# Optimization experiments

Hardware: AMD Instinct MI355X
Metric: run time of the kernel (lower is better)

Reference implementation:

```python
import jax, jax.numpy as jnp
import numpy as np

N, E, F_IN, H, L, G, C = 50000, 640000, 128, 128, 3, 256, 10
NEG_SLOPE = 0.2  # PyG GATConv default leaky_relu slope


def setup_inputs() -> dict:
    key = jax.random.key(0)
    ks = jax.random.split(key, 10)
    x = jax.random.normal(ks[0], (N, F_IN), jnp.float32)
    edge_index = jax.random.randint(ks[1], (2, E), 0, N, dtype=jnp.int32)
    # sorted graph ids covering all G graphs (global_max_pool segments)
    batch = (jnp.arange(N, dtype=jnp.int32) * G) // N
    s = 1.0 / np.sqrt(H)
    # 3 GAT layers all map 128->128 (F_IN == H), so stack their params
    Wc = jax.random.normal(ks[2], (L, F_IN, H), jnp.float32) * s
    a_src = jax.random.normal(ks[3], (L, H), jnp.float32) * s
    a_dst = jax.random.normal(ks[4], (L, H), jnp.float32) * s
    bc = jnp.zeros((L, H), jnp.float32)
    W1 = jax.random.normal(ks[5], (H, H), jnp.float32) * s
    b1 = jnp.zeros((H,), jnp.float32)
    W2 = jax.random.normal(ks[6], (H, C), jnp.float32) * s
    b2 = jnp.zeros((C,), jnp.float32)
    return dict(x=x, edge_index=edge_index, batch=batch, Wc=Wc, a_src=a_src,
                a_dst=a_dst, bc=bc, W1=W1, b1=b1, W2=W2, b2=b2)


def _gat_layer(h_in, W, a_s, a_d, b, src, dst):
    h = h_in @ W                                   # [N, H]
    e_s = (h * a_s).sum(-1)                        # [N] source term
    e_d = (h * a_d).sum(-1)                        # [N] target term
    e = jax.nn.leaky_relu(e_s[src] + e_d[dst], NEG_SLOPE)  # [E']
    # softmax over incoming edges of each target node
    m = jax.ops.segment_max(e, dst, num_segments=N)
    w = jnp.exp(e - m[dst])
    z = jax.ops.segment_sum(w, dst, num_segments=N)
    alpha = w / (z[dst] + 1e-16)
    out = jax.ops.segment_sum(alpha[:, None] * h[src], dst, num_segments=N)
    return out + b


def reference(x, edge_index, batch, Wc, a_src, a_dst, bc, W1, b1, W2, b2):
    loops = jnp.arange(N, dtype=edge_index.dtype)  # GATConv adds self-loops
    src = jnp.concatenate([edge_index[0], loops])
    dst = jnp.concatenate([edge_index[1], loops])
    h = x
    for l in range(L):
        h = jax.nn.relu(_gat_layer(h, Wc[l], a_src[l], a_dst[l], bc[l], src, dst))
    g = jax.ops.segment_max(h, batch, num_segments=G)  # global_max_pool [G, H]
    g = jax.nn.relu(g @ W1 + b1)
    logits = g @ W2 + b2
    return jax.nn.log_softmax(logits, axis=-1)
```

## Files before the change

### kernel.cpp

```cpp
#include <hip/hip_runtime.h>
#include <hip/hip_fp16.h>
#include <math.h>

#define N_ 50000
#define E_ 640000
#define H_ 128
#define L_ 3
#define G_ 256
#define C_ 10
#define NEG_SLOPE 0.2f

#define ABLK ((N_ + 3) / 4)
#define MAXDEG 64
#define GEMM_BLKS ((N_ + 63) / 64)
#define FILL_T (GEMM_BLKS * 256)

typedef _Float16 half8 __attribute__((ext_vector_type(8)));
typedef float f32x4 __attribute__((ext_vector_type(4)));

__device__ __forceinline__ float leaky(float x) { return x > 0.f ? x : NEG_SLOPE * x; }
__device__ __forceinline__ int pi_out(int p) { return ((p & 7) << 4) + (p >> 3); }

__device__ __forceinline__ void prep_layer(int l, const float* __restrict__ Wc,
                                           const float* __restrict__ a_src,
                                           const float* __restrict__ a_dst,
                                           const float* __restrict__ bc,
                                           __half* __restrict__ Wt,
                                           float* __restrict__ bcp) {
    const float* W = Wc + l * 16384;
    __half* T = Wt + (size_t)l * 144 * 128;
    int t = threadIdx.x;
    for (int e = t; e < 16384; e += 256) {
        int n = e >> 7, p = e & 127;
        int ks = (l == 0) ? p : pi_out(p);
        T[n * 128 + p] = __float2half(W[ks * 128 + n]);
    }
    if (t < 128) {
        int p = t;
        int ks = (l == 0) ? p : pi_out(p);
        const float* as = a_src + l * 128;
        const float* ad = a_dst + l * 128;
        float s = 0.f, d = 0.f;
#pragma unroll 8
        for (int n = 0; n < 128; n++) {
            float w = W[ks * 128 + n];
            s += w * as[n];
            d += w * ad[n];
        }
        T[128 * 128 + p] = __float2half(s);
        T[129 * 128 + p] = __float2half(d);
        bcp[l * 128 + p] = bc[l * 128 + pi_out(p)];
    } else {
        int kk = t - 128;
        for (int r = 130; r < 144; r++) T[r * 128 + kk] = __float2half(0.f);
    }
}

__global__ __launch_bounds__(256) void zero_prep(int* __restrict__ cur,
                                                 const float* __restrict__ Wc,
                                                 const float* __restrict__ a_src,
                                                 const float* __restrict__ a_dst,
                                                 const float* __restrict__ bc,
                                                 __half* __restrict__ Wt,
                                                 float* __restrict__ bcp) {
    if (blockIdx.x < L_) {
        prep_layer(blockIdx.x, Wc, a_src, a_dst, bc, Wt, bcp);
    } else {
        int i = (blockIdx.x - L_) * 256 + threadIdx.x;
        if (i < N_) cur[i] = 0;
    }
}

__global__ __launch_bounds__(256) void gemm0_fill(const float* __restrict__ A,
                                                  const __half* __restrict__ Wt,
                                                  __half* __restrict__ h16,
                                                  float* __restrict__ es,
                                                  float* __restrict__ ed,
                                                  const int* __restrict__ src,
                                                  const int* __restrict__ dst,
                                                  int* __restrict__ cur,
                                                  int* __restrict__ col_slots) {
    __shared__ __half Bsw[144 * 128];
    int tid = threadIdx.x;
    int brow = blockIdx.x * 64;
    int w = tid >> 6, l = tid & 63;
    int lrow = l & 15, lk = l >> 4;

    int g = blockIdx.x * 256 + tid;
    int e1 = g + FILL_T, e2 = g + 2 * FILL_T, e3 = g + 3 * FILL_T;
    bool v3 = e3 < E_;
    int d0 = dst[g], d1 = dst[e1], d2 = dst[e2];
    int s0 = src[g], s1 = src[e1], s2 = src[e2];
    int d3 = 0, s3 = 0;
    if (v3) { d3 = dst[e3]; s3 = src[e3]; }

    int p0 = atomicAdd(&cur[d0], 1);
    int p1 = atomicAdd(&cur[d1], 1);
    int p2 = atomicAdd(&cur[d2], 1);
    int p3 = MAXDEG;
    if (v3) p3 = atomicAdd(&cur[d3], 1);

    int arow = brow + w * 16 + lrow;
    float4 av[8];
    if (arow < N_) {
        const float4* rp = (const float4*)(A + (size_t)arow * 128);
#pragma unroll
        for (int kk = 0; kk < 4; kk++) {
            av[2 * kk]     = rp[kk * 8 + lk * 2];
            av[2 * kk + 1] = rp[kk * 8 + lk * 2 + 1];
        }
    } else {
        float4 zz = make_float4(0.f, 0.f, 0.f, 0.f);
#pragma unroll
        for (int s = 0; s < 8; s++) av[s] = zz;
    }

    {
        const float4* srcW = (const float4*)Wt;
#pragma unroll
        for (int i = 0; i < 9; i++) {
            int c = tid + i * 256;
            int o = c * 16;
            int n = o >> 8;
            float4 val = srcW[c];
            int addr = n * 256 + ((o & 255) ^ ((n & 7) << 4));
            *(float4*)((char*)Bsw + addr) = val;
        }
    }
    __syncthreads();

    f32x4 acc[9];
#pragma unroll
    for (int t = 0; t < 9; t++) acc[t] = (f32x4)0.f;
#pragma unroll
    for (int kk = 0; kk < 4; kk++) {
        half8 af;
        float4 a0 = av[2 * kk], a1 = av[2 * kk + 1];
        af[0] = (_Float16)a0.x; af[1] = (_Float16)a0.y; af[2] = (_Float16)a0.z; af[3] = (_Float16)a0.w;
        af[4] = (_Float16)a1.x; af[5] = (_Float16)a1.y; af[6] = (_Float16)a1.z; af[7] = (_Float16)a1.w;
        int kbyte = kk * 64 + lk * 16;
#pragma unroll
        for (int t = 0; t < 9; t++) {
            int n = t * 16 + lrow;
            half8 bf = *(const half8*)((const char*)Bsw + n * 256 + (kbyte ^ ((n & 7) << 4)));
            acc[t] = __builtin_amdgcn_mfma_f32_16x16x32_f16(af, bf, acc[t], 0, 0, 0);
        }
    }

    int row0 = brow + w * 16 + lk * 4;
#pragma unroll
    for (int rr = 0; rr < 4; rr++) {
        int gr = row0 + rr;
        if (gr < N_) {
            half8 hv;
#pragma unroll
            for (int t = 0; t < 8; t++) hv[t] = (_Float16)acc[t][rr];
            *(half8*)(h16 + (size_t)gr * 128 + lrow * 8) = hv;
            if (lrow == 0) es[gr] = acc[8][rr];
            else if (lrow == 1) ed[gr] = acc[8][rr];
        }
    }

    if (p0 < MAXDEG) col_slots[d0 * MAXDEG + p0] = s0;
    if (p1 < MAXDEG) col_slots[d1 * MAXDEG + p1] = s1;
    if (p2 < MAXDEG) col_slots[d2 * MAXDEG + p2] = s2;
    if (p3 < MAXDEG) col_slots[d3 * MAXDEG + p3] = s3;
}

__global__ __launch_bounds__(256) void gemm_mfma(const __half* __restrict__ Ah,
                                                 const __half* __restrict__ Wt,
                                                 __half* __restrict__ h16,
                                                 float* __restrict__ es,
                                                 float* __restrict__ ed) {
    __shared__ __half Bsw[144 * 128];
    int tid = threadIdx.x;
    int brow = blockIdx.x * 64;
    int w = tid >> 6, l = tid & 63;
    int lrow = l & 15, lk = l >> 4;

    int arow = brow + w * 16 + lrow;
    half8 afr[4];
    if (arow < N_) {
        const char* rb = (const char*)(Ah + (size_t)arow * 128);
#pragma unroll
        for (int kk = 0; kk < 4; kk++)
            afr[kk] = *(const half8*)(rb + kk * 64 + lk * 16);
    } else {
#pragma unroll
        for (int kk = 0; kk < 4; kk++) afr[kk] = (half8)(_Float16)0.f;
    }

    {
        const float4* srcW = (const float4*)Wt;
#pragma unroll
        for (int i = 0; i < 9; i++) {
            int c = tid + i * 256;
            int o = c * 16;
            int n = o >> 8;
            float4 val = srcW[c];
            int addr = n * 256 + ((o & 255) ^ ((n & 7) << 4));
            *(float4*)((char*)Bsw + addr) = val;
        }
    }
    __syncthreads();

    f32x4 acc[9];
#pragma unroll
    for (int t = 0; t < 9; t++) acc[t] = (f32x4)0.f;
#pragma unroll
    for (int kk = 0; kk < 4; kk++) {
        int kbyte = kk * 64 + lk * 16;
#pragma unroll
        for (int t = 0; t < 9; t++) {
            int n = t * 16 + lrow;
            half8 bf = *(const half8*)((const char*)Bsw + n * 256 + (kbyte ^ ((n & 7) << 4)));
            acc[t] = __builtin_amdgcn_mfma_f32_16x16x32_f16(afr[kk], bf, acc[t], 0, 0, 0);
        }
    }

    int row0 = brow + w * 16 + lk * 4;
#pragma unroll
    for (int rr = 0; rr < 4; rr++) {
        int gr = row0 + rr;
        if (gr < N_) {
            half8 hv;
#pragma unroll
            for (int t = 0; t < 8; t++) hv[t] = (_Float16)acc[t][rr];
            *(half8*)(h16 + (size_t)gr * 128 + lrow * 8) = hv;
            if (lrow == 0) es[gr] = acc[8][rr];
            else if (lrow == 1) ed[gr] = acc[8][rr];
        }
    }
}

__global__ __launch_bounds__(256) void gat_aggregate(const __half* __restrict__ h16,
                                                     const float* __restrict__ es,
                                                     const float* __restrict__ ed,
                                                     const int* __restrict__ cur,
                                                     const int* __restrict__ col_slots,
                                                     const float* __restrict__ biasp,
                                                     __half* __restrict__ hout) {
    __shared__ int   lds_s[4][64];
    __shared__ float lds_w[4][64];
    int wv = threadIdx.x >> 6;
    int lane = threadIdx.x & 63;
    int node = blockIdx.x * 4 + wv;
    if (node >= N_) return;

    int deg_raw = cur[node];
    int craw = col_slots[node * MAXDEG + lane];
    float edn = ed[node];
    float es_self = es[node];

    int deg = min(deg_raw, MAXDEG);
    int c0 = (lane < deg) ? min(max(craw, 0), N_ - 1) : node;
    lds_s[wv][lane] = c0;

    float w0 = 0.f;
    if (lane < deg) w0 = __expf(fminf(leaky(es[c0] + edn), 30.f));
    float zl = w0;
    lds_w[wv][lane] = w0;

    int eg = lane >> 4;
    int fl = lane & 15;

    float acc[8] = {0.f, 0.f, 0.f, 0.f, 0.f, 0.f, 0.f, 0.f};
    int K4 = (deg + 15) >> 4;
    for (int b = 0; b < K4; ++b) {
        int jb = eg + (b << 4);
        int s0 = lds_s[wv][jb];
        int s1 = lds_s[wv][jb + 4];
        int s2 = lds_s[wv][jb + 8];
        int s3 = lds_s[wv][jb + 12];
        float a0 = lds_w[wv][jb];
        float a1 = lds_w[wv][jb + 4];
        float a2 = lds_w[wv][jb + 8];
        float a3 = lds_w[wv][jb + 12];
        union { float4 f4; __half2 h2[4]; } u0, u1, u2, u3;
        u0.f4 = *(const float4*)(h16 + (size_t)s0 * 128 + fl * 8);
        u1.f4 = *(const float4*)(h16 + (size_t)s1 * 128 + fl * 8);
        u2.f4 = *(const float4*)(h16 + (size_t)s2 * 128 + fl * 8);
        u3.f4 = *(const float4*)(h16 + (size_t)s3 * 128 + fl * 8);
#pragma unroll
        for (int qq = 0; qq < 4; qq++) {
            float2 f0 = __half22float2(u0.h2[qq]);
            float2 f1 = __half22float2(u1.h2[qq]);
            float2 f2 = __half22float2(u2.h2[qq]);
            float2 f3 = __half22float2(u3.h2[qq]);
            acc[2 * qq]     += a0 * f0.x + a1 * f1.x + a2 * f2.x + a3 * f3.x;
            acc[2 * qq + 1] += a0 * f0.y + a1 * f1.y + a2 * f2.y + a3 * f3.y;
        }
    }

#pragma unroll
    for (int qq = 0; qq < 8; qq++) {
        acc[qq] += __shfl_xor(acc[qq], 16);
        acc[qq] += __shfl_xor(acc[qq], 32);
    }
#pragma unroll
    for (int o = 32; o; o >>= 1) zl += __shfl_xor(zl, o);
    float ws = __expf(fminf(leaky(es_self + edn), 30.f));
    float inv = 1.0f / (zl + ws + 1e-16f);

    if (eg == 0) {
        union { float4 f4; __half2 h2[4]; } su;
        su.f4 = *(const float4*)(h16 + (size_t)node * 128 + fl * 8);
        const float4* bp = (const float4*)(biasp + fl * 8);
        float4 b0 = bp[0], b1 = bp[1];
        float bq[8] = {b0.x, b0.y, b0.z, b0.w, b1.x, b1.y, b1.z, b1.w};
        union { float4 f4; __half2 h2[4]; } ou;
#pragma unroll
        for (int qq = 0; qq < 4; qq++) {
            float2 sv = __half22float2(su.h2[qq]);
            float v0 = fmaxf((acc[2 * qq]     + ws * sv.x) * inv + bq[2 * qq],     0.f);
            float v1 = fmaxf((acc[2 * qq + 1] + ws * sv.y) * inv + bq[2 * qq + 1], 0.f);
            ou.h2[qq] = __floats2half2_rn(v0, v1);
        }
        *(float4*)(hout + (size_t)node * 128 + fl * 8) = ou.f4;
    }
}

__device__ __forceinline__ int lower_bound_batch(const int* __restrict__ batch, int val) {
    int lo = 0, hi = N_;
    while (lo < hi) {
        int mid = (lo + hi) >> 1;
        if (batch[mid] < val) lo = mid + 1;
        else hi = mid;
    }
    return lo;
}

__global__ __launch_bounds__(512) void pool_head(const __half* __restrict__ h16,
                                                 const int* __restrict__ batch,
                                                 const float* __restrict__ W1,
                                                 const float* __restrict__ b1,
                                                 const float* __restrict__ W2,
                                                 const float* __restrict__ b2,
                                                 float* __restrict__ out) {
    int g = blockIdx.x;
    int t = threadIdx.x;
    __shared__ float red[8][128];
    __shared__ float gs[128], gp[128], lg[C_], lse;

    int s = lower_bound_batch(batch, g);
    int e = lower_bound_batch(batch, g + 1);
    int fs = t & 15;
    int rg = t >> 4;
    float m[8] = {0.f, 0.f, 0.f, 0.f, 0.f, 0.f, 0.f, 0.f};
    for (int i = s + rg; i < e; i += 32) {
        union { float4 f4; __half2 h2[4]; } u;
        u.f4 = *(const float4*)(h16 + (size_t)i * 128 + fs * 8);
#pragma unroll
        for (int qq = 0; qq < 4; qq++) {
            float2 fv = __half22float2(u.h2[qq]);
            m[2 * qq]     = fmaxf(m[2 * qq],     fv.x);
            m[2 * qq + 1] = fmaxf(m[2 * qq + 1], fv.y);
        }
    }
#pragma unroll
    for (int qq = 0; qq < 8; qq++) {
        m[qq] = fmaxf(m[qq], __shfl_xor(m[qq], 16));
        m[qq] = fmaxf(m[qq], __shfl_xor(m[qq], 32));
    }
    int wid = t >> 6;
    if ((t & 48) == 0) {
#pragma unroll
        for (int qq = 0; qq < 8; qq++) red[wid][fs * 8 + qq] = m[qq];
    }
    __syncthreads();
    if (t < 128) {
        float mm = red[0][t];
#pragma unroll
        for (int w = 1; w < 8; w++) mm = fmaxf(mm, red[w][t]);
        gs[t] = mm;
    }
    __syncthreads();

    if (t < 128) {
        float acc = b1[t];
#pragma unroll 8
        for (int k = 0; k < 128; k++) {
            int f = pi_out(k);
            acc += gs[k] * W1[f * 128 + t];
        }
        gp[t] = fmaxf(acc, 0.f);
    }
    __syncthreads();
    if (t < C_) {
        float a2 = b2[t];
#pragma unroll 8
        for (int k = 0; k < 128; k++) a2 += gp[k] * W2[k * C_ + t];
        lg[t] = a2;
    }
    __syncthreads();
    if (t == 0) {
        float mm = lg[0];
#pragma unroll
        for (int i = 1; i < C_; i++) mm = fmaxf(mm, lg[i]);
        float ss = 0.f;
#pragma unroll
        for (int i = 0; i < C_; i++) ss += expf(lg[i] - mm);
        lse = mm + logf(ss);
    }
    __syncthreads();
    if (t < C_) out[g * C_ + t] = lg[t] - lse;
}

extern "C" void kernel_launch(void* const* d_in, const int* in_sizes, int n_in,
                              void* d_out, int out_size, void* d_ws, size_t ws_size,
                              hipStream_t stream) {
    const float* x     = (const float*)d_in[0];
    const int*   eidx  = (const int*)d_in[1];
    const int*   batch = (const int*)d_in[2];
    const float* Wc    = (const float*)d_in[3];
    const float* a_src = (const float*)d_in[4];
    const float* a_dst = (const float*)d_in[5];
    const float* bc    = (const float*)d_in[6];
    const float* W1    = (const float*)d_in[7];
    const float* b1    = (const float*)d_in[8];
    const float* W2    = (const float*)d_in[9];
    const float* b2    = (const float*)d_in[10];
    float* out = (float*)d_out;

    const int* srcs = eidx;
    const int* dsts = eidx + E_;

    __half* hG16  = (__half*)d_ws;
    __half* hB16  = hG16 + (size_t)N_ * 128;
    float*  es    = (float*)(hB16 + (size_t)N_ * 128);
    float*  ed    = es + N_;
    float*  bcp   = ed + N_;
    __half* Wt    = (__half*)(bcp + 3 * 128);
    int*    cur       = (int*)(Wt + (size_t)3 * 144 * 128);
    int*    col_slots = cur + N_;

    zero_prep<<<L_ + (N_ + 255) / 256, 256, 0, stream>>>(cur, Wc, a_src, a_dst, bc, Wt, bcp);

    gemm0_fill<<<GEMM_BLKS, 256, 0, stream>>>(x, Wt, hG16, es, ed,
                                              srcs, dsts, cur, col_slots);

    gat_aggregate<<<ABLK, 256, 0, stream>>>(hG16, es, ed, cur, col_slots, bcp, hB16);
    for (int l = 1; l < L_; ++l) {
        gemm_mfma<<<GEMM_BLKS, 256, 0, stream>>>(
            hB16, Wt + (size_t)l * 144 * 128, hG16, es, ed);
        gat_aggregate<<<ABLK, 256, 0, stream>>>(hG16, es, ed, cur, col_slots,
                                                bcp + l * 128, hB16);
    }

    pool_head<<<G_, 512, 0, stream>>>(hB16, batch, W1, b1, W2, b2, out);
}
```

Baseline: 186.0 us.

## Fuse GAT aggregation with next layer's MFMA GEMM via LDS tile

Layers 0 and 1 now run their edge-softmax aggregation (plus bias and ReLU) inside the following layer's GEMM kernel. Each 64-node tile is aggregated into LDS, then multiplied by the next weight matrix with MFMA. This removes a global write and read of the intermediate fp16 activations and one kernel launch per fused pair. The es/ed buffers are double-buffered so one launch can read the old attention terms while writing the new ones. The cost is fewer, heavier blocks (64 nodes each instead of 4) and more LDS use, which may lower occupancy for the gather-heavy phase.

```diff
diff --git a/kernel.cpp b/kernel.cpp
--- a/kernel.cpp
+++ b/kernel.cpp
@@ -167,31 +167,25 @@
     if (p3 < MAXDEG) col_slots[d3 * MAXDEG + p3] = s3;
 }
 
-__global__ __launch_bounds__(256) void gemm_mfma(const __half* __restrict__ Ah,
-                                                 const __half* __restrict__ Wt,
-                                                 __half* __restrict__ h16,
-                                                 float* __restrict__ es,
-                                                 float* __restrict__ ed) {
+__global__ __launch_bounds__(256) void agg_gemm(const __half* __restrict__ gin,
+                                                const float* __restrict__ es_in,
+                                                const float* __restrict__ ed_in,
+                                                const int* __restrict__ cur,
+                                                const int* __restrict__ col_slots,
+                                                const float* __restrict__ biasp,
+                                                const __half* __restrict__ Wt_l,
+                                                __half* __restrict__ gout,
+                                                float* __restrict__ es_out,
+                                                float* __restrict__ ed_out) {
+    __shared__ __half Asw[64 * 128];
     __shared__ __half Bsw[144 * 128];
     int tid = threadIdx.x;
     int brow = blockIdx.x * 64;
-    int w = tid >> 6, l = tid & 63;
-    int lrow = l & 15, lk = l >> 4;
-
-    int arow = brow + w * 16 + lrow;
-    half8 afr[4];
-    if (arow < N_) {
-        const char* rb = (const char*)(Ah + (size_t)arow * 128);
-#pragma unroll
-        for (int kk = 0; kk < 4; kk++)
-            afr[kk] = *(const half8*)(rb + kk * 64 + lk * 16);
-    } else {
-#pragma unroll
-        for (int kk = 0; kk < 4; kk++) afr[kk] = (half8)(_Float16)0.f;
-    }
+    int w = tid >> 6, lane = tid & 63;
+    int eg = lane >> 4, fl = lane & 15;
 
     {
-        const float4* srcW = (const float4*)Wt;
+        const float4* srcW = (const float4*)Wt_l;
 #pragma unroll
         for (int i = 0; i < 9; i++) {
             int c = tid + i * 256;
@@ -202,19 +196,94 @@
             *(float4*)((char*)Bsw + addr) = val;
         }
     }
-    __syncthreads();
-
-    f32x4 acc[9];
-#pragma unroll
-    for (int t = 0; t < 9; t++) acc[t] = (f32x4)0.f;
+
+    for (int nt = 0; nt < 16; ++nt) {
+        int nl = w * 16 + nt;
+        int node = brow + nl;
+        int wr_addr = nl * 256 + ((fl * 16) ^ ((nl & 7) << 4));
+        if (node >= N_) {
+            if (eg == 0) *(float4*)((char*)Asw + wr_addr) = make_float4(0.f, 0.f, 0.f, 0.f);
+            continue;
+        }
+        int deg = min(cur[node], MAXDEG);
+        int craw = col_slots[node * MAXDEG + lane];
+        float edn = ed_in[node];
+        float es_self = es_in[node];
+        int c0 = (lane < deg) ? min(max(craw, 0), N_ - 1) : node;
+        float w0 = 0.f;
+        if (lane < deg) w0 = __expf(fminf(leaky(es_in[c0] + edn), 30.f));
+        float zl = w0;
+
+        float acc[8] = {0.f, 0.f, 0.f, 0.f, 0.f, 0.f, 0.f, 0.f};
+#pragma unroll
+        for (int b = 0; b < 4; ++b) {
+            int jb = eg + (b << 4);
+            int s0 = __shfl(c0, jb);
+            int s1 = __shfl(c0, jb + 4);
+            int s2 = __shfl(c0, jb + 8);
+            int s3 = __shfl(c0, jb + 12);
+            float a0 = __shfl(w0, jb);
+            float a1 = __shfl(w0, jb + 4);
+            float a2 = __shfl(w0, jb + 8);
+            float a3 = __shfl(w0, jb + 12);
+            union { float4 f4; __half2 h2[4]; } u0, u1, u2, u3;
+            u0.f4 = *(const float4*)(gin + (size_t)s0 * 128 + fl * 8);
+            u1.f4 = *(const float4*)(gin + (size_t)s1 * 128 + fl * 8);
+            u2.f4 = *(const float4*)(gin + (size_t)s2 * 128 + fl * 8);
+            u3.f4 = *(const float4*)(gin + (size_t)s3 * 128 + fl * 8);
+#pragma unroll
+            for (int qq = 0; qq < 4; qq++) {
+                float2 f0 = __half22float2(u0.h2[qq]);
+                float2 f1 = __half22float2(u1.h2[qq]);
+                float2 f2 = __half22float2(u2.h2[qq]);
+                float2 f3 = __half22float2(u3.h2[qq]);
+                acc[2 * qq]     += a0 * f0.x + a1 * f1.x + a2 * f2.x + a3 * f3.x;
+                acc[2 * qq + 1] += a0 * f0.y + a1 * f1.y + a2 * f2.y + a3 * f3.y;
+            }
+        }
+#pragma unroll
+        for (int qq = 0; qq < 8; qq++) {
+            acc[qq] += __shfl_xor(acc[qq], 16);
+            acc[qq] += __shfl_xor(acc[qq], 32);
+        }
+#pragma unroll
+        for (int o = 32; o; o >>= 1) zl += __shfl_xor(zl, o);
+        float ws = __expf(fminf(leaky(es_self + edn), 30.f));
+        float inv = 1.0f / (zl + ws + 1e-16f);
+
+        if (eg == 0) {
+            union { float4 f4; __half2 h2[4]; } su;
+            su.f4 = *(const float4*)(gin + (size_t)node * 128 + fl * 8);
+            const float4* bp = (const float4*)(biasp + fl * 8);
+            float4 b0 = bp[0], b1 = bp[1];
+            float bq[8] = {b0.x, b0.y, b0.z, b0.w, b1.x, b1.y, b1.z, b1.w};
+            union { float4 f4; __half2 h2[4]; } ou;
+#pragma unroll
+            for (int qq = 0; qq < 4; qq++) {
+                float2 sv = __half22float2(su.h2[qq]);
+                float v0 = fmaxf((acc[2 * qq]     + ws * sv.x) * inv + bq[2 * qq],     0.f);
+                float v1 = fmaxf((acc[2 * qq + 1] + ws * sv.y) * inv + bq[2 * qq + 1], 0.f);
+                ou.h2[qq] = __floats2half2_rn(v0, v1);
+            }
+            *(float4*)((char*)Asw + wr_addr) = ou.f4;
+        }
+    }
+    __syncthreads();
+
+    int lrow = lane & 15, lk = lane >> 4;
+    f32x4 acc2[9];
+#pragma unroll
+    for (int t = 0; t < 9; t++) acc2[t] = (f32x4)0.f;
 #pragma unroll
     for (int kk = 0; kk < 4; kk++) {
         int kbyte = kk * 64 + lk * 16;
+        int ar = w * 16 + lrow;
+        half8 af = *(const half8*)((const char*)Asw + ar * 256 + (kbyte ^ ((ar & 7) << 4)));
 #pragma unroll
         for (int t = 0; t < 9; t++) {
             int n = t * 16 + lrow;
             half8 bf = *(const half8*)((const char*)Bsw + n * 256 + (kbyte ^ ((n & 7) << 4)));
-            acc[t] = __builtin_amdgcn_mfma_f32_16x16x32_f16(afr[kk], bf, acc[t], 0, 0, 0);
+            acc2[t] = __builtin_amdgcn_mfma_f32_16x16x32_f16(af, bf, acc2[t], 0, 0, 0);
         }
     }
 
@@ -225,10 +294,10 @@
         if (gr < N_) {
             half8 hv;
 #pragma unroll
-            for (int t = 0; t < 8; t++) hv[t] = (_Float16)acc[t][rr];
-            *(half8*)(h16 + (size_t)gr * 128 + lrow * 8) = hv;
-            if (lrow == 0) es[gr] = acc[8][rr];
-            else if (lrow == 1) ed[gr] = acc[8][rr];
+            for (int t = 0; t < 8; t++) hv[t] = (_Float16)acc2[t][rr];
+            *(half8*)(gout + (size_t)gr * 128 + lrow * 8) = hv;
+            if (lrow == 0) es_out[gr] = acc2[8][rr];
+            else if (lrow == 1) ed_out[gr] = acc2[8][rr];
         }
     }
 }
@@ -425,27 +494,31 @@
     const int* srcs = eidx;
     const int* dsts = eidx + E_;
 
-    __half* hG16  = (__half*)d_ws;
-    __half* hB16  = hG16 + (size_t)N_ * 128;
-    float*  es    = (float*)(hB16 + (size_t)N_ * 128);
-    float*  ed    = es + N_;
-    float*  bcp   = ed + N_;
+    __half* hA    = (__half*)d_ws;
+    __half* hB    = hA + (size_t)N_ * 128;
+    float*  esA   = (float*)(hB + (size_t)N_ * 128);
+    float*  edA   = esA + N_;
+    float*  esB   = edA + N_;
+    float*  edB   = esB + N_;
+    float*  bcp   = edB + N_;
     __half* Wt    = (__half*)(bcp + 3 * 128);
     int*    cur       = (int*)(Wt + (size_t)3 * 144 * 128);
     int*    col_slots = cur + N_;
 
     zero_prep<<<L_ + (N_ + 255) / 256, 256, 0, stream>>>(cur, Wc, a_src, a_dst, bc, Wt, bcp);
 
-    gemm0_fill<<<GEMM_BLKS, 256, 0, stream>>>(x, Wt, hG16, es, ed,
+    gemm0_fill<<<GEMM_BLKS, 256, 0, stream>>>(x, Wt, hA, esA, edA,
                                               srcs, dsts, cur, col_slots);
 
-    gat_aggregate<<<ABLK, 256, 0, stream>>>(hG16, es, ed, cur, col_slots, bcp, hB16);
-    for (int l = 1; l < L_; ++l) {
-        gemm_mfma<<<GEMM_BLKS, 256, 0, stream>>>(
-            hB16, Wt + (size_t)l * 144 * 128, hG16, es, ed);
-        gat_aggregate<<<ABLK, 256, 0, stream>>>(hG16, es, ed, cur, col_slots,
-                                                bcp + l * 128, hB16);
-    }
-
-    pool_head<<<G_, 512, 0, stream>>>(hB16, batch, W1, b1, W2, b2, out);
-}
+    agg_gemm<<<GEMM_BLKS, 256, 0, stream>>>(hA, esA, edA, cur, col_slots,
+                                            bcp, Wt + (size_t)1 * 144 * 128,
+                                            hB, esB, edB);
+    agg_gemm<<<GEMM_BLKS, 256, 0, stream>>>(hB, esB, edB, cur, col_slots,
+                                            bcp + 128, Wt + (size_t)2 * 144 * 128,
+                                            hA, esA, edA);
+
+    gat_aggregate<<<ABLK, 256, 0, stream>>>(hA, esA, edA, cur, col_slots,
+                                            bcp + 256, hB);
+
+    pool_head<<<G_, 512, 0, stream>>>(hB, batch, W1, b1, W2, b2, out);
+}
```

After: 271.2 us. 1.46x slower.
